# Optimization experiments

Hardware: AMD Instinct MI355X
Metric: run time of the kernel (lower is better)

## Reference

```python
import jax, jax.numpy as jnp
import numpy as np

N, F, H, C = 50000, 128, 4, 32   # nodes, in_channels, heads, hidden_channels
E, R, DE = 800000, 8, 64         # edges, num_relations, edge_dim


def setup_inputs() -> dict:
    key = jax.random.key(0)
    ks = jax.random.split(key, 10)
    x = jax.random.normal(ks[0], (N, F), dtype=jnp.float32)
    edge_index = jax.random.randint(ks[1], (2, E), 0, N, dtype=jnp.int64)
    edge_type = jax.random.randint(ks[2], (E,), 0, R, dtype=jnp.int64)
    s_in = 1.0 / np.sqrt(F)
    s_e = 1.0 / np.sqrt(DE)
    edge_emb = jax.random.normal(ks[3], (R, DE), dtype=jnp.float32)
    Wq = jax.random.normal(ks[4], (F, H * C), dtype=jnp.float32) * s_in
    Wk = jax.random.normal(ks[5], (F, H * C), dtype=jnp.float32) * s_in
    Wv = jax.random.normal(ks[6], (F, H * C), dtype=jnp.float32) * s_in
    We = jax.random.normal(ks[7], (DE, H * C), dtype=jnp.float32) * s_e
    Wskip = jax.random.normal(ks[8], (F, H * C), dtype=jnp.float32) * s_in
    return {"x": x, "edge_index": edge_index, "edge_type": edge_type,
            "edge_emb": edge_emb, "Wq": Wq, "Wk": Wk, "Wv": Wv,
            "We": We, "Wskip": Wskip}


def reference(x, edge_index, edge_type, edge_emb, Wq, Wk, Wv, We, Wskip):
    # TransformerConv (PyG) with edge embeddings, concat heads, root skip, no bias.
    src, dst = edge_index[0], edge_index[1]
    q = (x @ Wq).reshape(N, H, C)
    k = (x @ Wk).reshape(N, H, C)
    v = (x @ Wv).reshape(N, H, C)
    e = (edge_emb[edge_type] @ We).reshape(E, H, C)      # per-edge relation emb
    kj = k[src] + e                                       # [E,H,C]
    logits = (q[dst] * kj).sum(-1) / jnp.sqrt(jnp.float32(C))  # [E,H]
    # segment softmax over incoming edges of each target node
    m = jax.ops.segment_max(logits, dst, num_segments=N)  # [N,H]
    m = jnp.where(jnp.isfinite(m), m, jnp.float32(0.0))
    ex = jnp.exp(logits - m[dst])
    denom = jax.ops.segment_sum(ex, dst, num_segments=N)  # [N,H]
    alpha = ex / (denom[dst] + 1e-16)                     # [E,H]
    msg = (v[src] + e) * alpha[:, :, None]                # [E,H,C]
    out = jax.ops.segment_sum(msg, dst, num_segments=N).reshape(N, H * C)
    return out + x @ Wskip
```

## Files before the change

kernel.cpp:

```cpp
#include <hip/hip_runtime.h>
#include <hip/hip_bf16.h>

#define NN 50000
#define FF 128
#define NH 4
#define CH 32
#define HC 128
#define NE 800000
#define NR 8
#define DEDIM 64
#define PBLK 98
#define QKB 625
#define MTILES 3125
#define CAP 48

typedef __hip_bfloat16 bf16;
typedef __attribute__((ext_vector_type(8))) short short8;
typedef __attribute__((ext_vector_type(4))) float f32x4;

__device__ __forceinline__ float bflo(unsigned u) { return __uint_as_float(u << 16); }
__device__ __forceinline__ float bfhi(unsigned u) { return __uint_as_float(u & 0xFFFF0000u); }

__device__ __forceinline__ unsigned short f2bf(float f) {
  unsigned u = __float_as_uint(f);
  unsigned r = (u + 0x7FFFu + ((u >> 16) & 1u)) >> 16;
  return (unsigned short)r;
}
__device__ __forceinline__ unsigned pack2bf(float lo, float hi) {
  return (unsigned)f2bf(lo) | ((unsigned)f2bf(hi) << 16);
}

__device__ __forceinline__ void ldsbar() {
  asm volatile("s_waitcnt lgkmcnt(0)\n\ts_barrier" ::: "memory");
}

template <int ISBF>
__device__ __forceinline__ float ldf(const void* p, size_t i) {
  if (ISBF) return __bfloat162float(((const bf16*)p)[i]);
  return ((const float*)p)[i];
}

__global__ __launch_bounds__(256) void k_wt(const unsigned* __restrict__ xw,
    const void* __restrict__ Wq, const void* __restrict__ Ws,
    const void* __restrict__ Wk, const void* __restrict__ Wv,
    unsigned short* __restrict__ wtr, int* __restrict__ hist) {
  unsigned ex = (xw[threadIdx.x & 63] >> 7) & 0xFFu;
  unsigned long long bb = __ballot(ex < 90u || ex > 140u);
  int isbf = (bb == 0ULL);
  int i = blockIdx.x * 256 + threadIdx.x;
  int m = i >> 14, n = (i >> 7) & 127, k = i & 127;
  const void* W = (m == 0) ? Wq : (m == 1) ? Ws : (m == 2) ? Wk : Wv;
  wtr[i] = isbf ? ((const unsigned short*)W)[k * HC + n]
                : f2bf(((const float*)W)[k * HC + n]);
  if (i < NN) hist[i] = 0;
}

template <int ISBF>
__device__ __forceinline__ void qkvs4_body(const void* __restrict__ x,
    const unsigned short* __restrict__ wtr,
    unsigned short* __restrict__ qb, unsigned* __restrict__ kvb,
    void* __restrict__ out, unsigned char* __restrict__ est, int mc) {
  const int tid  = threadIdx.x;
  const int lane = tid & 63;
  const int wv   = tid >> 6;
  const int quad = lane >> 4;
  const int lr   = lane & 15;
  short8 bf[4][2][4];
#pragma unroll
  for (int m = 0; m < 4; ++m)
#pragma unroll
    for (int t = 0; t < 2; ++t) {
      int ncol = wv * 32 + t * 16 + lr;
#pragma unroll
      for (int kb = 0; kb < 4; ++kb)
        bf[m][t][kb] = *(const short8*)&wtr[(m * HC + ncol) * FF + kb * 32 + quad * 8];
    }
  unsigned short* qs  = (unsigned short*)est;
  unsigned short* sbs = (unsigned short*)(est + 4096);
  float*          sfs = (float*)(est + 4096);
  unsigned*       kvs = (unsigned*)est;
  const unsigned short* xu = (const unsigned short*)x;
  const float* xf = (const float*)x;
  short8 lda[4];
  float4 raw[8];
  {
    size_t off = (size_t)(mc * 16 + lr) * FF + quad * 8;
    if (ISBF) {
#pragma unroll
      for (int kb = 0; kb < 4; ++kb) lda[kb] = *(const short8*)(xu + off + kb * 32);
    } else {
#pragma unroll
      for (int kb = 0; kb < 4; ++kb) {
        raw[2 * kb]     = *(const float4*)(xf + off + kb * 32);
        raw[2 * kb + 1] = *(const float4*)(xf + off + kb * 32 + 4);
      }
    }
  }
  for (int mt = mc; mt < MTILES; mt += QKB) {
    int m0 = mt * 16;
    short8 cur[4];
    if (ISBF) {
#pragma unroll
      for (int kb = 0; kb < 4; ++kb) cur[kb] = lda[kb];
    } else {
#pragma unroll
      for (int kb = 0; kb < 4; ++kb) {
        float4 a = raw[2 * kb], b = raw[2 * kb + 1];
        short8 o;
        o[0] = (short)f2bf(a.x); o[1] = (short)f2bf(a.y);
        o[2] = (short)f2bf(a.z); o[3] = (short)f2bf(a.w);
        o[4] = (short)f2bf(b.x); o[5] = (short)f2bf(b.y);
        o[6] = (short)f2bf(b.z); o[7] = (short)f2bf(b.w);
        cur[kb] = o;
      }
    }
    int mtn = mt + QKB;
    if (mtn < MTILES) {
      size_t off = (size_t)(mtn * 16 + lr) * FF + quad * 8;
      if (ISBF) {
#pragma unroll
        for (int kb = 0; kb < 4; ++kb) lda[kb] = *(const short8*)(xu + off + kb * 32);
      } else {
#pragma unroll
        for (int kb = 0; kb < 4; ++kb) {
          raw[2 * kb]     = *(const float4*)(xf + off + kb * 32);
          raw[2 * kb + 1] = *(const float4*)(xf + off + kb * 32 + 4);
        }
      }
    }
    f32x4 acc[4][2];
#pragma unroll
    for (int m = 0; m < 4; ++m)
#pragma unroll
      for (int t = 0; t < 2; ++t) acc[m][t] = {0.f, 0.f, 0.f, 0.f};
#pragma unroll
    for (int kb = 0; kb < 4; ++kb)
#pragma unroll
      for (int m = 0; m < 4; ++m) {
        acc[m][0] = __builtin_amdgcn_mfma_f32_16x16x32_bf16(cur[kb], bf[m][0][kb], acc[m][0], 0, 0, 0);
        acc[m][1] = __builtin_amdgcn_mfma_f32_16x16x32_bf16(cur[kb], bf[m][1][kb], acc[m][1], 0, 0, 0);
      }
#pragma unroll
    for (int t = 0; t < 2; ++t)
#pragma unroll
      for (int r = 0; r < 4; ++r) {
        int li = (quad * 4 + r) * HC + wv * 32 + t * 16 + lr;
        qs[li] = f2bf(acc[0][t][r]);
        if (ISBF) sbs[li] = f2bf(acc[1][t][r]);
        else      sfs[li] = acc[1][t][r];
      }
    ldsbar();
    {
      int row = tid >> 4, seg = tid & 15;
      *(uint4*)(qb + (size_t)(m0 + row) * HC + seg * 8) = ((const uint4*)qs)[tid];
      if (ISBF) {
        *(uint4*)((unsigned short*)out + (size_t)(m0 + row) * HC + seg * 8) =
            ((const uint4*)sbs)[tid];
      } else {
#pragma unroll
        for (int s = 0; s < 2; ++s) {
          int idx = s * 256 + tid, rw = idx >> 5, sg = idx & 31;
          *(uint4*)((float*)out + (size_t)(m0 + rw) * HC + sg * 4) =
              ((const uint4*)sfs)[idx];
        }
      }
    }
    ldsbar();
#pragma unroll
    for (int t = 0; t < 2; ++t)
#pragma unroll
      for (int r = 0; r < 4; ++r) {
        int li = (quad * 4 + r) * HC + wv * 32 + t * 16 + lr;
        kvs[li] = pack2bf(acc[2][t][r], acc[3][t][r]);
      }
    ldsbar();
#pragma unroll
    for (int s = 0; s < 2; ++s) {
      int idx = s * 256 + tid, rw = idx >> 5, sg = idx & 31;
      *(uint4*)(kvb + (size_t)(m0 + rw) * HC + sg * 4) = ((const uint4*)kvs)[idx];
    }
    ldsbar();
  }
}

__global__ __launch_bounds__(256) void k_fused(const unsigned* __restrict__ xw,
    const int* __restrict__ eidx32, const void* __restrict__ etype,
    const void* __restrict__ emb, const void* __restrict__ We,
    const unsigned short* __restrict__ wtr,
    int* __restrict__ flag, int* __restrict__ hist, float* __restrict__ ee,
    int* __restrict__ bucket,
    unsigned short* __restrict__ qb, unsigned* __restrict__ kvb,
    void* __restrict__ out) {
  __shared__ __align__(16) unsigned char shm[12288];
  if (blockIdx.x < PBLK) {
    unsigned long long b = __ballot(eidx32[2 * (threadIdx.x & 63) + 1] != 0);
    int is64 = (b == 0ULL);
    int ebase = (blockIdx.x * 256 + threadIdx.x) * 32;
    if (ebase >= NE) return;
#pragma unroll
    for (int c = 0; c < 4; ++c) {
      int e0 = ebase + c * 8;
      int src[8], dst[8], et[8];
      if (is64) {
        const int4* p4 = (const int4*)eidx32;
        const int4* t4 = (const int4*)etype;
#pragma unroll
        for (int j = 0; j < 4; ++j) {
          int4 a = p4[(e0 >> 1) + j];
          int4 cc = p4[((NE + e0) >> 1) + j];
          int4 t0 = t4[(e0 >> 1) + j];
          src[2 * j] = a.x;  src[2 * j + 1] = a.z;
          dst[2 * j] = cc.x; dst[2 * j + 1] = cc.z;
          et[2 * j]  = t0.x; et[2 * j + 1]  = t0.z;
        }
      } else {
        const int4* p4 = (const int4*)eidx32;
        const int4* t4 = (const int4*)etype;
#pragma unroll
        for (int j = 0; j < 2; ++j) {
          int4 a = p4[(e0 >> 2) + j];
          int4 cc = p4[((NE + e0) >> 2) + j];
          int4 t0 = t4[(e0 >> 2) + j];
          src[4 * j] = a.x; src[4 * j + 1] = a.y; src[4 * j + 2] = a.z; src[4 * j + 3] = a.w;
          dst[4 * j] = cc.x; dst[4 * j + 1] = cc.y; dst[4 * j + 2] = cc.z; dst[4 * j + 3] = cc.w;
          et[4 * j]  = t0.x; et[4 * j + 1] = t0.y; et[4 * j + 2] = t0.z; et[4 * j + 3] = t0.w;
        }
      }
      int rank[8];
#pragma unroll
      for (int u = 0; u < 8; ++u) {
        int dd = min(max(dst[u], 0), NN - 1);
        dst[u] = dd;
        rank[u] = atomicAdd(&hist[dd], 1);
      }
#pragma unroll
      for (int u = 0; u < 8; ++u) {
        int s  = min(max(src[u], 0), NN - 1);
        int tt = min(max(et[u], 0), NR - 1);
        int rk = min(rank[u], CAP - 1);
        bucket[dst[u] * CAP + rk] = (s << 3) | tt;
      }
    }
    return;
  }
  if (blockIdx.x < PBLK + QKB) {
    unsigned ex = (xw[threadIdx.x & 63] >> 7) & 0xFFu;
    unsigned long long bb = __ballot(ex < 90u || ex > 140u);
    int isbf = (bb == 0ULL);
    int mc = blockIdx.x - PBLK;
    if (isbf) qkvs4_body<1>(xw, wtr, qb, kvb, out, shm, mc);
    else      qkvs4_body<0>(xw, wtr, qb, kvb, out, shm, mc);
    return;
  }
  float* es = (float*)shm;
  __shared__ int nzIdx, badBf;
  if (threadIdx.x == 0) { nzIdx = 0; badBf = 0; }
  __syncthreads();
  if (threadIdx.x < 128) {
    if (eidx32[2 * threadIdx.x + 1] != 0) atomicAdd(&nzIdx, 1);
    unsigned e = (xw[threadIdx.x] >> 7) & 0xFFu;
    if (e < 90u || e > 140u) atomicAdd(&badBf, 1);
  }
  __syncthreads();
  const int isbf = (badBf == 0);
  if (threadIdx.x == 0) { flag[0] = (nzIdx == 0); flag[1] = isbf; }
  for (int i = threadIdx.x; i < NR * DEDIM; i += 256)
    es[i] = isbf ? ldf<1>(emb, i) : ldf<0>(emb, i);
  __syncthreads();
  for (int o = threadIdx.x; o < NR * HC; o += 256) {
    int r = o >> 7, j = o & 127;
    float acc = 0.f;
    if (isbf) { for (int d = 0; d < DEDIM; ++d) acc += es[r * DEDIM + d] * ldf<1>(We, d * HC + j); }
    else      { for (int d = 0; d < DEDIM; ++d) acc += es[r * DEDIM + d] * ldf<0>(We, d * HC + j); }
    ee[o] = acc;
  }
}

__global__ __launch_bounds__(256) void k_gather(const int* __restrict__ hist,
    const int* __restrict__ bucket, const unsigned short* __restrict__ qb,
    const unsigned* __restrict__ kvb, const float* __restrict__ ee,
    const int* __restrict__ flag, void* __restrict__ out) {
  int n = blockIdx.x * 4 + (threadIdx.x >> 6);
  int l = threadIdx.x & 63;
  int t = l >> 5;
  int w = l & 31;
  int j0 = ((w >> 3) << 5) + ((w & 7) << 2);
  int end = min(__builtin_amdgcn_readfirstlane(hist[n]), CAP);
  const int* row = bucket + n * CAP;
  uint2 qw = *(const uint2*)(qb + (size_t)n * HC + j0);
  float q0 = bflo(qw.x), q1 = bfhi(qw.x), q2 = bflo(qw.y), q3 = bfhi(qw.y);
  const float sc = 0.17677669529663687f;
  float dn = 0.f, a0 = 0.f, a1 = 0.f, a2 = 0.f, a3 = 0.f;
  int p = 0;
  for (; p + 8 <= end; p += 8) {
    int se[4]; uint4 kv[4]; float4 ev[4];
#pragma unroll
    for (int u = 0; u < 4; ++u) se[u] = row[p + 2 * u + t];
#pragma unroll
    for (int u = 0; u < 4; ++u)
      kv[u] = *(const uint4*)(kvb + (size_t)(se[u] >> 3) * HC + j0);
#pragma unroll
    for (int u = 0; u < 4; ++u)
      ev[u] = *(const float4*)(ee + ((se[u] & 7) << 7) + j0);
#pragma unroll
    for (int u = 0; u < 4; ++u) {
      float pp = q0 * (bflo(kv[u].x) + ev[u].x) + q1 * (bflo(kv[u].y) + ev[u].y)
               + q2 * (bflo(kv[u].z) + ev[u].z) + q3 * (bflo(kv[u].w) + ev[u].w);
      pp += __shfl_xor(pp, 1);
      pp += __shfl_xor(pp, 2);
      pp += __shfl_xor(pp, 4);
      float xx = __expf(pp * sc);
      dn += xx;
      a0 += (bfhi(kv[u].x) + ev[u].x) * xx;
      a1 += (bfhi(kv[u].y) + ev[u].y) * xx;
      a2 += (bfhi(kv[u].z) + ev[u].z) * xx;
      a3 += (bfhi(kv[u].w) + ev[u].w) * xx;
    }
  }
  if (p < end) {
    int se[4]; bool ok[4]; uint4 kv[4]; float4 ev[4];
#pragma unroll
    for (int u = 0; u < 4; ++u) {
      int pe = p + 2 * u + t;
      ok[u] = pe < end;
      se[u] = row[ok[u] ? pe : 0];
    }
#pragma unroll
    for (int u = 0; u < 4; ++u)
      kv[u] = *(const uint4*)(kvb + (size_t)(se[u] >> 3) * HC + j0);
#pragma unroll
    for (int u = 0; u < 4; ++u)
      ev[u] = *(const float4*)(ee + ((se[u] & 7) << 7) + j0);
#pragma unroll
    for (int u = 0; u < 4; ++u) {
      float pp = q0 * (bflo(kv[u].x) + ev[u].x) + q1 * (bflo(kv[u].y) + ev[u].y)
               + q2 * (bflo(kv[u].z) + ev[u].z) + q3 * (bflo(kv[u].w) + ev[u].w);
      pp += __shfl_xor(pp, 1);
      pp += __shfl_xor(pp, 2);
      pp += __shfl_xor(pp, 4);
      float xx = ok[u] ? __expf(pp * sc) : 0.f;
      dn += xx;
      a0 += (bfhi(kv[u].x) + ev[u].x) * xx;
      a1 += (bfhi(kv[u].y) + ev[u].y) * xx;
      a2 += (bfhi(kv[u].z) + ev[u].z) * xx;
      a3 += (bfhi(kv[u].w) + ev[u].w) * xx;
    }
  }
  dn += __shfl_xor(dn, 32);
  a0 += __shfl_xor(a0, 32);
  a1 += __shfl_xor(a1, 32);
  a2 += __shfl_xor(a2, 32);
  a3 += __shfl_xor(a3, 32);
  if (t == 0) {
    float inv = 1.f / (dn + 1e-16f);
    size_t oi = (size_t)n * HC + j0;
    if (flag[1]) {
      uint2 sk = *(const uint2*)((const unsigned short*)out + oi);
      uint2 o;
      o.x = pack2bf(a0 * inv + bflo(sk.x), a1 * inv + bfhi(sk.x));
      o.y = pack2bf(a2 * inv + bflo(sk.y), a3 * inv + bfhi(sk.y));
      *(uint2*)((unsigned short*)out + oi) = o;
    } else {
      float4 sk = *(const float4*)((const float*)out + oi);
      float4 o = make_float4(a0 * inv + sk.x, a1 * inv + sk.y,
                             a2 * inv + sk.z, a3 * inv + sk.w);
      *(float4*)((float*)out + oi) = o;
    }
  }
}

extern "C" void kernel_launch(void* const* d_in, const int* in_sizes, int n_in,
                              void* d_out, int out_size, void* d_ws, size_t ws_size,
                              hipStream_t stream) {
  const void* x     = d_in[0];
  const void* eidx  = d_in[1];
  const void* etype = d_in[2];
  const void* emb   = d_in[3];
  const void* Wq    = d_in[4];
  const void* Wk    = d_in[5];
  const void* Wv    = d_in[6];
  const void* We    = d_in[7];
  const void* Ws    = d_in[8];

  float* base   = (float*)d_ws;
  int*   flag   = (int*)base;
  float* ee     = base + 16;
  unsigned short* wtr = (unsigned short*)(base + 1040);
  int*   hist   = (int*)(base + 33824);
  int*   bucket = (int*)(base + 83840);
  unsigned short* qb  = (unsigned short*)(base + 2483840);
  unsigned*       kvb = (unsigned*)(base + 5683840);

  k_wt    <<<256, 256, 0, stream>>>((const unsigned*)x, Wq, Ws, Wk, Wv,
                                    wtr, hist);
  k_fused <<<PBLK + QKB + 1, 256, 0, stream>>>((const unsigned*)x,
                                               (const int*)eidx, etype, emb, We,
                                               wtr, flag, hist, ee, bucket,
                                               qb, kvb, d_out);
  k_gather<<<NN / 4, 256, 0, stream>>>(hist, bucket, qb, kvb, ee, flag, d_out);
}
```

Baseline: 213.3 us.

## Split fused bucketing/QKV kernel into separate launches and move edge-embedding prep

Breaks the heterogeneous fused kernel (edge bucketing blocks, QKV/skip GEMM blocks, edge-embedding block) into separate kernels: the edge-embedding and flag computation move into the weight-transpose kernel as an extra block, bucketing gets its own kernel with 16 edges per inner batch, and the GEMM gets its own kernel. The aim is to stop the slow atomic bucketing blocks from sharing a launch with the GEMM blocks and to give each kernel uniform resources. The cost is an extra kernel launch and the loss of overlap between bucketing and the GEMM within one grid.

```diff
diff --git a/kernel.cpp b/kernel.cpp
--- a/kernel.cpp
+++ b/kernel.cpp
@@ -41,18 +41,99 @@
 }
 
 __global__ __launch_bounds__(256) void k_wt(const unsigned* __restrict__ xw,
+    const int* __restrict__ eidx32, const void* __restrict__ emb,
+    const void* __restrict__ We,
     const void* __restrict__ Wq, const void* __restrict__ Ws,
     const void* __restrict__ Wk, const void* __restrict__ Wv,
-    unsigned short* __restrict__ wtr, int* __restrict__ hist) {
+    unsigned short* __restrict__ wtr, int* __restrict__ hist,
+    int* __restrict__ flag, float* __restrict__ ee) {
+  __shared__ float es[NR * DEDIM];
+  __shared__ int nzIdx, badBf;
   unsigned ex = (xw[threadIdx.x & 63] >> 7) & 0xFFu;
   unsigned long long bb = __ballot(ex < 90u || ex > 140u);
-  int isbf = (bb == 0ULL);
+  int isbfw = (bb == 0ULL);
   int i = blockIdx.x * 256 + threadIdx.x;
-  int m = i >> 14, n = (i >> 7) & 127, k = i & 127;
-  const void* W = (m == 0) ? Wq : (m == 1) ? Ws : (m == 2) ? Wk : Wv;
-  wtr[i] = isbf ? ((const unsigned short*)W)[k * HC + n]
-                : f2bf(((const float*)W)[k * HC + n]);
-  if (i < NN) hist[i] = 0;
+  if (blockIdx.x < 256) {
+    int m = i >> 14, n = (i >> 7) & 127, k = i & 127;
+    const void* W = (m == 0) ? Wq : (m == 1) ? Ws : (m == 2) ? Wk : Wv;
+    wtr[i] = isbfw ? ((const unsigned short*)W)[k * HC + n]
+                   : f2bf(((const float*)W)[k * HC + n]);
+    if (i < NN) hist[i] = 0;
+    return;
+  }
+  if (threadIdx.x == 0) { nzIdx = 0; badBf = 0; }
+  __syncthreads();
+  if (threadIdx.x < 128) {
+    if (eidx32[2 * threadIdx.x + 1] != 0) atomicAdd(&nzIdx, 1);
+    unsigned e = (xw[threadIdx.x] >> 7) & 0xFFu;
+    if (e < 90u || e > 140u) atomicAdd(&badBf, 1);
+  }
+  __syncthreads();
+  const int isbf = (badBf == 0);
+  if (threadIdx.x == 0) { flag[0] = (nzIdx == 0); flag[1] = isbf; }
+  for (int j = threadIdx.x; j < NR * DEDIM; j += 256)
+    es[j] = isbf ? ldf<1>(emb, j) : ldf<0>(emb, j);
+  __syncthreads();
+  for (int o = threadIdx.x; o < NR * HC; o += 256) {
+    int r = o >> 7, j = o & 127;
+    float acc = 0.f;
+    if (isbf) { for (int d = 0; d < DEDIM; ++d) acc += es[r * DEDIM + d] * ldf<1>(We, d * HC + j); }
+    else      { for (int d = 0; d < DEDIM; ++d) acc += es[r * DEDIM + d] * ldf<0>(We, d * HC + j); }
+    ee[o] = acc;
+  }
+}
+
+__global__ __launch_bounds__(256) void k_prep(const int* __restrict__ eidx32,
+    const void* __restrict__ etype, int* __restrict__ hist,
+    int* __restrict__ bucket) {
+  unsigned long long b = __ballot(eidx32[2 * (threadIdx.x & 63) + 1] != 0);
+  int is64 = (b == 0ULL);
+  int ebase = (blockIdx.x * 256 + threadIdx.x) * 32;
+  if (ebase >= NE) return;
+#pragma unroll
+  for (int c = 0; c < 2; ++c) {
+    int e0 = ebase + c * 16;
+    int src[16], dst[16], et[16];
+    if (is64) {
+      const int4* p4 = (const int4*)eidx32;
+      const int4* t4 = (const int4*)etype;
+#pragma unroll
+      for (int j = 0; j < 8; ++j) {
+        int4 a = p4[(e0 >> 1) + j];
+        int4 cc = p4[((NE + e0) >> 1) + j];
+        int4 t0 = t4[(e0 >> 1) + j];
+        src[2 * j] = a.x;  src[2 * j + 1] = a.z;
+        dst[2 * j] = cc.x; dst[2 * j + 1] = cc.z;
+        et[2 * j]  = t0.x; et[2 * j + 1]  = t0.z;
+      }
+    } else {
+      const int4* p4 = (const int4*)eidx32;
+      const int4* t4 = (const int4*)etype;
+#pragma unroll
+      for (int j = 0; j < 4; ++j) {
+        int4 a = p4[(e0 >> 2) + j];
+        int4 cc = p4[((NE + e0) >> 2) + j];
+        int4 t0 = t4[(e0 >> 2) + j];
+        src[4 * j] = a.x; src[4 * j + 1] = a.y; src[4 * j + 2] = a.z; src[4 * j + 3] = a.w;
+        dst[4 * j] = cc.x; dst[4 * j + 1] = cc.y; dst[4 * j + 2] = cc.z; dst[4 * j + 3] = cc.w;
+        et[4 * j]  = t0.x; et[4 * j + 1] = t0.y; et[4 * j + 2] = t0.z; et[4 * j + 3] = t0.w;
+      }
+    }
+    int rank[16];
+#pragma unroll
+    for (int u = 0; u < 16; ++u) {
+      int dd = min(max(dst[u], 0), NN - 1);
+      dst[u] = dd;
+      rank[u] = atomicAdd(&hist[dd], 1);
+    }
+#pragma unroll
+    for (int u = 0; u < 16; ++u) {
+      int s  = min(max(src[u], 0), NN - 1);
+      int tt = min(max(et[u], 0), NR - 1);
+      int rk = min(rank[u], CAP - 1);
+      bucket[dst[u] * CAP + rk] = (s << 3) | tt;
+    }
+  }
 }
 
 template <int ISBF>
@@ -183,97 +264,16 @@
   }
 }
 
-__global__ __launch_bounds__(256) void k_fused(const unsigned* __restrict__ xw,
-    const int* __restrict__ eidx32, const void* __restrict__ etype,
-    const void* __restrict__ emb, const void* __restrict__ We,
+__global__ __launch_bounds__(256) void k_qkvs(const unsigned* __restrict__ xw,
     const unsigned short* __restrict__ wtr,
-    int* __restrict__ flag, int* __restrict__ hist, float* __restrict__ ee,
-    int* __restrict__ bucket,
     unsigned short* __restrict__ qb, unsigned* __restrict__ kvb,
     void* __restrict__ out) {
-  __shared__ __align__(16) unsigned char shm[12288];
-  if (blockIdx.x < PBLK) {
-    unsigned long long b = __ballot(eidx32[2 * (threadIdx.x & 63) + 1] != 0);
-    int is64 = (b == 0ULL);
-    int ebase = (blockIdx.x * 256 + threadIdx.x) * 32;
-    if (ebase >= NE) return;
-#pragma unroll
-    for (int c = 0; c < 4; ++c) {
-      int e0 = ebase + c * 8;
-      int src[8], dst[8], et[8];
-      if (is64) {
-        const int4* p4 = (const int4*)eidx32;
-        const int4* t4 = (const int4*)etype;
-#pragma unroll
-        for (int j = 0; j < 4; ++j) {
-          int4 a = p4[(e0 >> 1) + j];
-          int4 cc = p4[((NE + e0) >> 1) + j];
-          int4 t0 = t4[(e0 >> 1) + j];
-          src[2 * j] = a.x;  src[2 * j + 1] = a.z;
-          dst[2 * j] = cc.x; dst[2 * j + 1] = cc.z;
-          et[2 * j]  = t0.x; et[2 * j + 1]  = t0.z;
-        }
-      } else {
-        const int4* p4 = (const int4*)eidx32;
-        const int4* t4 = (const int4*)etype;
-#pragma unroll
-        for (int j = 0; j < 2; ++j) {
-          int4 a = p4[(e0 >> 2) + j];
-          int4 cc = p4[((NE + e0) >> 2) + j];
-          int4 t0 = t4[(e0 >> 2) + j];
-          src[4 * j] = a.x; src[4 * j + 1] = a.y; src[4 * j + 2] = a.z; src[4 * j + 3] = a.w;
-          dst[4 * j] = cc.x; dst[4 * j + 1] = cc.y; dst[4 * j + 2] = cc.z; dst[4 * j + 3] = cc.w;
-          et[4 * j]  = t0.x; et[4 * j + 1] = t0.y; et[4 * j + 2] = t0.z; et[4 * j + 3] = t0.w;
-        }
-      }
-      int rank[8];
-#pragma unroll
-      for (int u = 0; u < 8; ++u) {
-        int dd = min(max(dst[u], 0), NN - 1);
-        dst[u] = dd;
-        rank[u] = atomicAdd(&hist[dd], 1);
-      }
-#pragma unroll
-      for (int u = 0; u < 8; ++u) {
-        int s  = min(max(src[u], 0), NN - 1);
-        int tt = min(max(et[u], 0), NR - 1);
-        int rk = min(rank[u], CAP - 1);
-        bucket[dst[u] * CAP + rk] = (s << 3) | tt;
-      }
-    }
-    return;
-  }
-  if (blockIdx.x < PBLK + QKB) {
-    unsigned ex = (xw[threadIdx.x & 63] >> 7) & 0xFFu;
-    unsigned long long bb = __ballot(ex < 90u || ex > 140u);
-    int isbf = (bb == 0ULL);
-    int mc = blockIdx.x - PBLK;
-    if (isbf) qkvs4_body<1>(xw, wtr, qb, kvb, out, shm, mc);
-    else      qkvs4_body<0>(xw, wtr, qb, kvb, out, shm, mc);
-    return;
-  }
-  float* es = (float*)shm;
-  __shared__ int nzIdx, badBf;
-  if (threadIdx.x == 0) { nzIdx = 0; badBf = 0; }
-  __syncthreads();
-  if (threadIdx.x < 128) {
-    if (eidx32[2 * threadIdx.x + 1] != 0) atomicAdd(&nzIdx, 1);
-    unsigned e = (xw[threadIdx.x] >> 7) & 0xFFu;
-    if (e < 90u || e > 140u) atomicAdd(&badBf, 1);
-  }
-  __syncthreads();
-  const int isbf = (badBf == 0);
-  if (threadIdx.x == 0) { flag[0] = (nzIdx == 0); flag[1] = isbf; }
-  for (int i = threadIdx.x; i < NR * DEDIM; i += 256)
-    es[i] = isbf ? ldf<1>(emb, i) : ldf<0>(emb, i);
-  __syncthreads();
-  for (int o = threadIdx.x; o < NR * HC; o += 256) {
-    int r = o >> 7, j = o & 127;
-    float acc = 0.f;
-    if (isbf) { for (int d = 0; d < DEDIM; ++d) acc += es[r * DEDIM + d] * ldf<1>(We, d * HC + j); }
-    else      { for (int d = 0; d < DEDIM; ++d) acc += es[r * DEDIM + d] * ldf<0>(We, d * HC + j); }
-    ee[o] = acc;
-  }
+  __shared__ __align__(16) unsigned char est[12288];
+  unsigned ex = (xw[threadIdx.x & 63] >> 7) & 0xFFu;
+  unsigned long long bb = __ballot(ex < 90u || ex > 140u);
+  int isbf = (bb == 0ULL);
+  if (isbf) qkvs4_body<1>(xw, wtr, qb, kvb, out, est, blockIdx.x);
+  else      qkvs4_body<0>(xw, wtr, qb, kvb, out, est, blockIdx.x);
 }
 
 __global__ __launch_bounds__(256) void k_gather(const int* __restrict__ hist,
@@ -391,11 +391,10 @@
   unsigned short* qb  = (unsigned short*)(base + 2483840);
   unsigned*       kvb = (unsigned*)(base + 5683840);
 
-  k_wt    <<<256, 256, 0, stream>>>((const unsigned*)x, Wq, Ws, Wk, Wv,
-                                    wtr, hist);
-  k_fused <<<PBLK + QKB + 1, 256, 0, stream>>>((const unsigned*)x,
-                                               (const int*)eidx, etype, emb, We,
-                                               wtr, flag, hist, ee, bucket,
-                                               qb, kvb, d_out);
+  k_wt    <<<257, 256, 0, stream>>>((const unsigned*)x, (const int*)eidx,
+                                    emb, We, Wq, Ws, Wk, Wv,
+                                    wtr, hist, flag, ee);
+  k_prep  <<<PBLK, 256, 0, stream>>>((const int*)eidx, etype, hist, bucket);
+  k_qkvs  <<<QKB, 256, 0, stream>>>((const unsigned*)x, wtr, qb, kvb, d_out);
   k_gather<<<NN / 4, 256, 0, stream>>>(hist, bucket, qb, kvb, ee, flag, d_out);
 }
```

Measured after the change: 257.5 us. 20.7% more time.
